# Kernel tuning notes

Measured on AMD Instinct MI355X. Metric: run time of the kernel, lower is better.

The kernel has to match this reference:

```python
import jax, jax.numpy as jnp
import numpy as np

SHIFT_MIN, SHIFT_MAX = -14.0, 0.0  # deepshift range for weight_bits=5: (-(2**4-2), 0)


def shift_quant(w):
    """Quantize weights to signed powers of two (bit-shift weights), STE form."""
    sign = jnp.sign(w)
    shift = jnp.clip(jnp.round(jnp.log2(jnp.abs(w) + 1e-12)), SHIFT_MIN, SHIFT_MAX)
    q = sign * jnp.exp2(shift)
    return w + jax.lax.stop_gradient(q - w)


def moe_fc(t, wg, w0, b0, w1, b1):
    """Top-1 routing over 2 experts: expert0 dense Linear, expert1 shift-quantized Linear.
    t: [T, C]; weights torch-layout [out, in]. With top_k=1 the softmaxed top-k gate is 1.0,
    so combine is a hard select of the chosen expert's output."""
    logits = t @ wg                      # [T, 2]
    pick0 = (jnp.argmax(logits, axis=-1) == 0)[:, None]
    y0 = t @ w0.T + b0                   # dense expert
    y1 = t @ shift_quant(w1).T + b1      # shift expert
    return jnp.where(pick0, y0, y1)


def setup_inputs() -> dict:
    key = jax.random.key(0)
    ks = jax.random.split(key, 10)
    B, N, C, Dh = 16, 1024, 512, 2048
    s = 0.02
    return {
        "x": jax.random.normal(ks[0], (B, N, C), jnp.float32),
        "H": 32,
        "W": 32,
        "wg1": jax.random.normal(ks[1], (C, 2), jnp.float32) * s,
        "fc1_w0": jax.random.normal(ks[2], (Dh, C), jnp.float32) * s,
        "fc1_b0": jnp.zeros((Dh,), jnp.float32),
        "fc1_w1": jax.random.normal(ks[3], (Dh, C), jnp.float32) * s,
        "fc1_b1": jnp.zeros((Dh,), jnp.float32),
        "dw_w": jax.random.normal(ks[4], (Dh, 1, 3, 3), jnp.float32) * np.sqrt(2.0 / 9.0),
        "dw_b": jnp.zeros((Dh,), jnp.float32),
        "wg2": jax.random.normal(ks[5], (Dh, 2), jnp.float32) * s,
        "fc2_w0": jax.random.normal(ks[6], (C, Dh), jnp.float32) * s,
        "fc2_b0": jnp.zeros((C,), jnp.float32),
        "fc2_w1": jax.random.normal(ks[7], (C, Dh), jnp.float32) * s,
        "fc2_b1": jnp.zeros((C,), jnp.float32),
    }


def reference(x, H, W, wg1, fc1_w0, fc1_b0, fc1_w1, fc1_b1, dw_w, dw_b,
              wg2, fc2_w0, fc2_b0, fc2_w1, fc2_b1):
    B, N, C = x.shape
    Dh = fc1_w0.shape[0]
    # fc1 MoE
    h = moe_fc(x.reshape(-1, C), wg1, fc1_w0, fc1_b0, fc1_w1, fc1_b1)  # [B*N, Dh]
    # DWConv 3x3 depthwise, NCHW
    h = h.reshape(B, N, Dh).transpose(0, 2, 1).reshape(B, Dh, H, W)
    h = jax.lax.conv_general_dilated(
        h, dw_w, window_strides=(1, 1), padding="SAME",
        dimension_numbers=("NCHW", "OIHW", "NCHW"), feature_group_count=Dh)
    h = h + dw_b[None, :, None, None]
    h = h.reshape(B, Dh, N).transpose(0, 2, 1)  # [B, N, Dh]
    # GELU (exact, as nn.GELU default); dropout p=0 -> identity
    h = jax.nn.gelu(h, approximate=False)
    # fc2 MoE
    y = moe_fc(h.reshape(-1, Dh), wg2, fc2_w0, fc2_b0, fc2_w1, fc2_b1)
    return y.reshape(B, N, -1)
```

## Files before the change

### kernel.cpp

```cpp
#include <hip/hip_runtime.h>
#include <hip/hip_bf16.h>


#define TOKS  16384
#define CIN   512
#define DHID  2048

typedef __attribute__((ext_vector_type(8))) __bf16 bf16x8;
typedef __attribute__((ext_vector_type(4))) float  f32x4;
typedef __attribute__((ext_vector_type(4))) float  float4v;
typedef __attribute__((ext_vector_type(4))) unsigned short ushort4v;

__device__ __forceinline__ unsigned short f2bf(float f) {
  union { float f; unsigned int u; } a; a.f = f;
  unsigned int u = a.u;
  unsigned int r = u + 0x7FFFu + ((u >> 16) & 1u);
  return (unsigned short)(r >> 16);
}
__device__ __forceinline__ float bf2f(unsigned short h) {
  union { unsigned int u; float f; } a; a.u = ((unsigned int)h) << 16;
  return a.f;
}

__device__ __forceinline__ float squant(float w) {
  if (w == 0.0f) return 0.0f;
  float aw = fabsf(w) + 1e-12f;
  union { float f; unsigned u; } a; a.f = aw;
  int e = (int)((a.u >> 23) & 0xFFu) - 127;
  unsigned frac = a.u & 0x7FFFFFu;
  int shift = e + (frac >= 0x3504F4u ? 1 : 0);
  shift = min(max(shift, -14), 0);
  union { unsigned u; float f; } q; q.u = (unsigned)(shift + 127) << 23;
  return (w > 0.0f) ? q.f : -q.f;
}

#define GLDS16(gp, lp) __builtin_amdgcn_global_load_lds(                      \
    (const __attribute__((address_space(1))) void*)(gp),                      \
    (__attribute__((address_space(3))) void*)(lp), 16, 0, 0)

__global__ void k_prep(const float* __restrict__ w0, const float* __restrict__ w1,
                       const float* __restrict__ w20, const float* __restrict__ w21,
                       unsigned short* __restrict__ w0hi, unsigned short* __restrict__ w0lo,
                       unsigned short* __restrict__ w1q, unsigned short* __restrict__ w20b,
                       unsigned short* __restrict__ w21b) {
  int i = blockIdx.x * 256 + threadIdx.x;
  if (i >= DHID * CIN) return;
  float v = w0[i];
  unsigned short h = f2bf(v);
  w0hi[i] = h;
  w0lo[i] = f2bf(v - bf2f(h));
  w1q[i]  = f2bf(squant(w1[i]));
  w20b[i] = f2bf(w20[i]);
  w21b[i] = f2bf(squant(w21[i]));
}

__global__ void k_prepx(const float* __restrict__ x,
                        unsigned short* __restrict__ xhi, unsigned short* __restrict__ xlo) {
  int i = blockIdx.x * 256 + threadIdx.x;
  float4v v = ((const float4v*)x)[i];
  ushort4v hv, lv;
  #pragma unroll
  for (int q = 0; q < 4; ++q) {
    unsigned short h = f2bf(v[q]);
    hv[q] = h;
    lv[q] = f2bf(v[q] - bf2f(h));
  }
  ((ushort4v*)xhi)[i] = hv;
  ((ushort4v*)xlo)[i] = lv;
}

__global__ void k_gate1(const float* __restrict__ x, const float* __restrict__ wg1,
                        unsigned char* __restrict__ pick1) {
  int tok = blockIdx.x * 4 + (threadIdx.x >> 6);
  int l = threadIdx.x & 63;
  const float* xr = x + (size_t)tok * CIN;
  float s0 = 0.f, s1 = 0.f;
  for (int i = l; i < CIN; i += 64) {
    float v = xr[i];
    s0 += v * wg1[i * 2 + 0];
    s1 += v * wg1[i * 2 + 1];
  }
  for (int m = 32; m; m >>= 1) { s0 += __shfl_xor(s0, m); s1 += __shfl_xor(s1, m); }
  if (l == 0) pick1[tok] = (s0 >= s1) ? 0 : 1;
}

__global__ void k_scan(const unsigned char* __restrict__ pick, int* __restrict__ perm,
                       int* __restrict__ n0buf) {
  __shared__ int cnt[1024];
  const int t = threadIdx.x;
  unsigned char loc[16];
  int c0 = 0;
  #pragma unroll
  for (int i = 0; i < 16; ++i) { loc[i] = pick[t * 16 + i]; c0 += (loc[i] == 0); }
  cnt[t] = c0;
  __syncthreads();
  for (int off = 1; off < 1024; off <<= 1) {
    int v = cnt[t] + ((t >= off) ? cnt[t - off] : 0);
    __syncthreads();
    cnt[t] = v;
    __syncthreads();
  }
  int total0 = cnt[1023];
  int pre0 = cnt[t] - c0;
  int pre1 = t * 16 - pre0;
  if (t == 0) n0buf[0] = total0;
  int p0 = pre0, p1 = total0 + pre1;
  #pragma unroll
  for (int i = 0; i < 16; ++i) {
    int tok = t * 16 + i;
    if (loc[i] == 0) perm[p0++] = tok; else perm[p1++] = tok;
  }
}

__launch_bounds__(256, 2)
__global__ void k_fc1(const unsigned short* __restrict__ xhi,
                      const unsigned short* __restrict__ xlo,
                      const unsigned short* __restrict__ w0hi,
                      const unsigned short* __restrict__ w0lo,
                      const unsigned short* __restrict__ w1q,
                      const float* __restrict__ b0, const float* __restrict__ b1,
                      const int* __restrict__ perm, const int* __restrict__ n0buf,
                      float* __restrict__ h32) {
  __shared__ unsigned short sm[40960];
  const int t = threadIdx.x, wv = t >> 6, ln = t & 63;
  const int lr = ln & 15, lg = ln >> 4;
  const int tok0 = blockIdx.x * 128, nbase = blockIdx.y * 128;
  const int wm = (wv >> 1) * 64, wn = (wv & 1) * 64;
  const int n0 = n0buf[0];
  const bool do0 = (tok0 < n0), do1 = (tok0 + 128 > n0);

  int par[2];
  #pragma unroll
  for (int s = 0; s < 2; ++s)
    par[s] = perm[tok0 + ((s * 4 + wv) << 4) + (ln >> 2)];

  const int swsrc = (((ln & 3) ^ ((ln >> 3) & 3)) << 3);
  const int swrd  = ((lg ^ ((lr >> 1) & 3)) << 3);

  f32x4 acc0[4][4], acc1[4][4];
  #pragma unroll
  for (int i = 0; i < 4; ++i)
    #pragma unroll
    for (int j = 0; j < 4; ++j) {
      acc0[i][j] = f32x4{0.f, 0.f, 0.f, 0.f};
      acc1[i][j] = f32x4{0.f, 0.f, 0.f, 0.f};
    }

  auto STAGE = [&](int kt, int db) {
    const int k0 = kt * 32;
    #pragma unroll
    for (int s = 0; s < 2; ++s) {
      const int rowblk = s * 4 + wv;
      const int aoff = db * 8192 + (rowblk << 9);
      const int boff = 16384 + db * 12288 + (rowblk << 9);
      size_t ga = (size_t)par[s] * CIN + k0 + swsrc;
      size_t gb = (size_t)(nbase + (rowblk << 4) + (ln >> 2)) * CIN + k0 + swsrc;
      GLDS16(xhi + ga, &sm[aoff]);
      GLDS16(xlo + ga, &sm[aoff + 4096]);
      GLDS16(w0hi + gb, &sm[boff]);
      GLDS16(w0lo + gb, &sm[boff + 4096]);
      GLDS16(w1q + gb, &sm[boff + 8192]);
    }
  };

  auto COMPUTE = [&](int db) {
    bf16x8 ah[4], al[4];
    #pragma unroll
    for (int mt = 0; mt < 4; ++mt) {
      int ro = (wm + (mt << 4) + lr) * 32 + swrd;
      ah[mt] = *(const bf16x8*)&sm[db * 8192 + ro];
      al[mt] = *(const bf16x8*)&sm[db * 8192 + 4096 + ro];
    }
    __builtin_amdgcn_s_setprio(1);
    #pragma unroll
    for (int nt = 0; nt < 4; ++nt) {
      int bb = 16384 + db * 12288 + (wn + (nt << 4) + lr) * 32 + swrd;
      if (do0) {
        bf16x8 bh = *(const bf16x8*)&sm[bb];
        bf16x8 bl = *(const bf16x8*)&sm[bb + 4096];
        #pragma unroll
        for (int mt = 0; mt < 4; ++mt) {
          acc0[mt][nt] = __builtin_amdgcn_mfma_f32_16x16x32_bf16(ah[mt], bh, acc0[mt][nt], 0, 0, 0);
          acc0[mt][nt] = __builtin_amdgcn_mfma_f32_16x16x32_bf16(al[mt], bh, acc0[mt][nt], 0, 0, 0);
          acc0[mt][nt] = __builtin_amdgcn_mfma_f32_16x16x32_bf16(ah[mt], bl, acc0[mt][nt], 0, 0, 0);
        }
      }
      if (do1) {
        bf16x8 bq = *(const bf16x8*)&sm[bb + 8192];
        #pragma unroll
        for (int mt = 0; mt < 4; ++mt) {
          acc1[mt][nt] = __builtin_amdgcn_mfma_f32_16x16x32_bf16(ah[mt], bq, acc1[mt][nt], 0, 0, 0);
          acc1[mt][nt] = __builtin_amdgcn_mfma_f32_16x16x32_bf16(al[mt], bq, acc1[mt][nt], 0, 0, 0);
        }
      }
    }
    __builtin_amdgcn_s_setprio(0);
  };

  STAGE(0, 0);
  #pragma unroll 2
  for (int kt = 0; kt < 15; ++kt) {
    __builtin_amdgcn_s_barrier();
    __builtin_amdgcn_sched_barrier(0);
    STAGE(kt + 1, (kt + 1) & 1);
    asm volatile("s_waitcnt vmcnt(10)" ::: "memory");
    __builtin_amdgcn_s_barrier();
    __builtin_amdgcn_sched_barrier(0);
    COMPUTE(kt & 1);
  }
  asm volatile("s_waitcnt vmcnt(0)" ::: "memory");
  __builtin_amdgcn_s_barrier();
  __builtin_amdgcn_sched_barrier(0);
  COMPUTE(1);

  #pragma unroll
  for (int nt = 0; nt < 4; ++nt) {
    int d = nbase + wn + (nt << 4) + lr;
    float bi0 = b0[d], bi1 = b1[d];
    #pragma unroll
    for (int mt = 0; mt < 4; ++mt) {
      f32x4 v0 = acc0[mt][nt], v1 = acc1[mt][nt];
      #pragma unroll
      for (int rr = 0; rr < 4; ++rr) {
        int pos = tok0 + wm + (mt << 4) + (lg << 2) + rr;
        int tok = perm[pos];
        float val = (pos >= n0) ? (v1[rr] + bi1) : (v0[rr] + bi0);
        h32[(size_t)tok * DHID + d] = val;
      }
    }
  }
}

__global__ void k_conv(const float* __restrict__ h32, const float* __restrict__ dww,
                       const float* __restrict__ dwb, const float* __restrict__ wg2,
                       unsigned short* __restrict__ hb, float* __restrict__ part) {
  __shared__ float tile[10][32][32];
  const int dc = blockIdx.x;
  const int ys = blockIdx.y;
  const int b  = blockIdx.z;
  const int t = threadIdx.x;
  const int d0 = dc * 32, y0 = ys * 8;

  for (int p = 0; p < 10240; p += 256) {
    int idx = p + t;
    int dl = idx & 31, xx = (idx >> 5) & 31, ry = idx >> 10;
    int y = y0 - 1 + ry;
    float v = 0.f;
    if (y >= 0 && y < 32)
      v = h32[(size_t)(b * 1024 + y * 32 + xx) * DHID + d0 + dl];
    tile[ry][xx][dl] = v;
  }
  __syncthreads();

  const int dl = t & 31, xg = t >> 5;
  const int d = d0 + dl;
  float kk[9];
  #pragma unroll
  for (int i = 0; i < 9; ++i) kk[i] = dww[d * 9 + i];
  const float bias = dwb[d];
  const float g0 = wg2[d * 2 + 0], g1 = wg2[d * 2 + 1];

  for (int yy = 0; yy < 8; ++yy) {
    int ry = yy + 1;
    #pragma unroll
    for (int xi = 0; xi < 4; ++xi) {
      int xx = xg * 4 + xi;
      float s = bias;
      #pragma unroll
      for (int dy = -1; dy <= 1; ++dy)
        #pragma unroll
        for (int dx = -1; dx <= 1; ++dx) {
          int xs = xx + dx;
          float v = (xs >= 0 && xs < 32) ? tile[ry + dy][xs][dl] : 0.f;
          s += v * kk[(dy + 1) * 3 + (dx + 1)];
        }
      float gg = 0.5f * s * (1.0f + erff(s * 0.70710678118654752f));
      int tok = b * 1024 + (y0 + yy) * 32 + xx;
      hb[(size_t)tok * DHID + d] = f2bf(gg);
      float p0 = gg * g0, p1 = gg * g1;
      for (int m = 16; m; m >>= 1) { p0 += __shfl_xor(p0, m); p1 += __shfl_xor(p1, m); }
      if (dl == 0) {
        part[(size_t)tok * 128 + dc] = p0;
        part[(size_t)tok * 128 + 64 + dc] = p1;
      }
    }
  }
}

__global__ void k_gate2(const float* __restrict__ part, unsigned char* __restrict__ pick2) {
  int tok = blockIdx.x * 4 + (threadIdx.x >> 6);
  int l = threadIdx.x & 63;
  const float* pr = part + (size_t)tok * 128;
  float s0 = pr[l], s1 = pr[64 + l];
  for (int m = 32; m; m >>= 1) { s0 += __shfl_xor(s0, m); s1 += __shfl_xor(s1, m); }
  if (l == 0) pick2[tok] = (s0 >= s1) ? 0 : 1;
}

__launch_bounds__(256, 2)
__global__ void k_fc2(const unsigned short* __restrict__ hb,
                      const unsigned short* __restrict__ w20b,
                      const unsigned short* __restrict__ w21b,
                      const float* __restrict__ b0, const float* __restrict__ b1,
                      const int* __restrict__ perm, const int* __restrict__ n0buf,
                      float* __restrict__ out) {
  __shared__ unsigned short sm[24576];
  const int t = threadIdx.x, wv = t >> 6, ln = t & 63;
  const int lr = ln & 15, lg = ln >> 4;
  const int tok0 = blockIdx.x * 128, nbase = blockIdx.y * 128;
  const int wm = (wv >> 1) * 64, wn = (wv & 1) * 64;
  const int n0 = n0buf[0];
  const bool do0 = (tok0 < n0), do1 = (tok0 + 128 > n0);

  int par[2];
  #pragma unroll
  for (int s = 0; s < 2; ++s)
    par[s] = perm[tok0 + ((s * 4 + wv) << 4) + (ln >> 2)];

  const int swsrc = (((ln & 3) ^ ((ln >> 3) & 3)) << 3);
  const int swrd  = ((lg ^ ((lr >> 1) & 3)) << 3);

  f32x4 acc0[4][4], acc1[4][4];
  #pragma unroll
  for (int i = 0; i < 4; ++i)
    #pragma unroll
    for (int j = 0; j < 4; ++j) {
      acc0[i][j] = f32x4{0.f, 0.f, 0.f, 0.f};
      acc1[i][j] = f32x4{0.f, 0.f, 0.f, 0.f};
    }

  auto STAGE = [&](int kt, int db) {
    const int k0 = kt * 32;
    #pragma unroll
    for (int s = 0; s < 2; ++s) {
      const int rowblk = s * 4 + wv;
      const int aoff = db * 4096 + (rowblk << 9);
      const int boff = 8192 + db * 8192 + (rowblk << 9);
      size_t ga = (size_t)par[s] * DHID + k0 + swsrc;
      size_t gb = (size_t)(nbase + (rowblk << 4) + (ln >> 2)) * DHID + k0 + swsrc;
      GLDS16(hb + ga, &sm[aoff]);
      GLDS16(w20b + gb, &sm[boff]);
      GLDS16(w21b + gb, &sm[boff + 4096]);
    }
  };

  auto COMPUTE = [&](int db) {
    bf16x8 a[4];
    #pragma unroll
    for (int mt = 0; mt < 4; ++mt)
      a[mt] = *(const bf16x8*)&sm[db * 4096 + (wm + (mt << 4) + lr) * 32 + swrd];
    __builtin_amdgcn_s_setprio(1);
    #pragma unroll
    for (int nt = 0; nt < 4; ++nt) {
      int bb = 8192 + db * 8192 + (wn + (nt << 4) + lr) * 32 + swrd;
      if (do0) {
        bf16x8 b0f = *(const bf16x8*)&sm[bb];
        #pragma unroll
        for (int mt = 0; mt < 4; ++mt)
          acc0[mt][nt] = __builtin_amdgcn_mfma_f32_16x16x32_bf16(a[mt], b0f, acc0[mt][nt], 0, 0, 0);
      }
      if (do1) {
        bf16x8 b1f = *(const bf16x8*)&sm[bb + 4096];
        #pragma unroll
        for (int mt = 0; mt < 4; ++mt)
          acc1[mt][nt] = __builtin_amdgcn_mfma_f32_16x16x32_bf16(a[mt], b1f, acc1[mt][nt], 0, 0, 0);
      }
    }
    __builtin_amdgcn_s_setprio(0);
  };

  STAGE(0, 0);
  #pragma unroll 2
  for (int kt = 0; kt < 63; ++kt) {
    __builtin_amdgcn_s_barrier();
    __builtin_amdgcn_sched_barrier(0);
    STAGE(kt + 1, (kt + 1) & 1);
    asm volatile("s_waitcnt vmcnt(6)" ::: "memory");
    __builtin_amdgcn_s_barrier();
    __builtin_amdgcn_sched_barrier(0);
    COMPUTE(kt & 1);
  }
  asm volatile("s_waitcnt vmcnt(0)" ::: "memory");
  __builtin_amdgcn_s_barrier();
  __builtin_amdgcn_sched_barrier(0);
  COMPUTE(1);

  #pragma unroll
  for (int nt = 0; nt < 4; ++nt) {
    int c = nbase + wn + (nt << 4) + lr;
    float bi0 = b0[c], bi1 = b1[c];
    #pragma unroll
    for (int mt = 0; mt < 4; ++mt) {
      f32x4 v0 = acc0[mt][nt], v1 = acc1[mt][nt];
      #pragma unroll
      for (int rr = 0; rr < 4; ++rr) {
        int pos = tok0 + wm + (mt << 4) + (lg << 2) + rr;
        int tok = perm[pos];
        float val = (pos >= n0) ? (v1[rr] + bi1) : (v0[rr] + bi0);
        out[(size_t)tok * CIN + c] = val;
      }
    }
  }
}

extern "C" void kernel_launch(void* const* d_in, const int* in_sizes, int n_in,
                              void* d_out, int out_size, void* d_ws, size_t ws_size,
                              hipStream_t stream) {
  (void)in_sizes; (void)n_in; (void)out_size; (void)ws_size;
  const float* x   = (const float*)d_in[0];
  const float* wg1 = (const float*)d_in[3];
  const float* w0  = (const float*)d_in[4];
  const float* b0  = (const float*)d_in[5];
  const float* w1  = (const float*)d_in[6];
  const float* b1  = (const float*)d_in[7];
  const float* dww = (const float*)d_in[8];
  const float* dwb = (const float*)d_in[9];
  const float* wg2 = (const float*)d_in[10];
  const float* w20 = (const float*)d_in[11];
  const float* b20 = (const float*)d_in[12];
  const float* w21 = (const float*)d_in[13];
  const float* b21 = (const float*)d_in[14];
  float* out = (float*)d_out;

  char* ws = (char*)d_ws;
  const size_t MB2 = 1u << 21;
  unsigned short* w0hi = (unsigned short*)(ws + 0 * MB2);
  unsigned short* w0lo = (unsigned short*)(ws + 1 * MB2);
  unsigned short* w1q  = (unsigned short*)(ws + 2 * MB2);
  unsigned short* w20b = (unsigned short*)(ws + 3 * MB2);
  unsigned short* w21b = (unsigned short*)(ws + 4 * MB2);
  char* p = ws + 5 * MB2;
  unsigned short* xhi = (unsigned short*)p;            p += (size_t)TOKS * CIN * 2;
  unsigned short* xlo = (unsigned short*)p;            p += (size_t)TOKS * CIN * 2;
  unsigned char* pick1 = (unsigned char*)p;            p += 65536;
  unsigned char* pick2 = (unsigned char*)p;            p += 65536;
  int* perm1 = (int*)p;                                p += TOKS * 4;
  int* perm2 = (int*)p;                                p += TOKS * 4;
  int* n0a   = (int*)p;                                p += 256;
  int* n0b   = (int*)p;                                p += 256;
  float* part = (float*)p;                             p += (size_t)TOKS * 128 * 4;
  float* h32  = (float*)p;                             p += (size_t)TOKS * DHID * 4;
  unsigned short* hb = (unsigned short*)p;

  k_prep <<<4096, 256, 0, stream>>>(w0, w1, w20, w21, w0hi, w0lo, w1q, w20b, w21b);
  k_prepx<<<8192, 256, 0, stream>>>(x, xhi, xlo);
  k_gate1<<<4096, 256, 0, stream>>>(x, wg1, pick1);
  k_scan <<<1, 1024, 0, stream>>>(pick1, perm1, n0a);
  k_fc1  <<<dim3(128, 16), 256, 0, stream>>>(xhi, xlo, w0hi, w0lo, w1q, b0, b1, perm1, n0a, h32);
  k_conv <<<dim3(64, 4, 16), 256, 0, stream>>>(h32, dww, dwb, wg2, hb, part);
  k_gate2<<<4096, 256, 0, stream>>>(part, pick2);
  k_scan <<<1, 1024, 0, stream>>>(pick2, perm2, n0b);
  k_fc2  <<<dim3(128, 4), 256, 0, stream>>>(hb, w20b, w21b, b20, b21, perm2, n0b, out);
}
```

Measured before the change: 441.7 us.

## Stage GEMM epilogues through LDS, vectorize conv, and swizzle block order

The fc1 and fc2 epilogues now write the accumulators into shared memory and read them back, so each row of scattered output goes to global memory as 16-byte vector stores instead of 4-byte strided scalar stores. The depthwise conv kernel is rewritten so each thread handles four channels, loading and storing them as float4 and bf16x4 vectors, and the gate partial reduction needs fewer shuffles. The GEMM grids become 1D with a grouped block ordering (8 token tiles per group) to improve L2 reuse of the weight tiles. This adds an extra LDS round trip and a __syncthreads in each epilogue.

```diff
diff --git a/kernel.cpp b/kernel.cpp
--- a/kernel.cpp
+++ b/kernel.cpp
@@ -124,7 +124,9 @@
   __shared__ unsigned short sm[40960];
   const int t = threadIdx.x, wv = t >> 6, ln = t & 63;
   const int lr = ln & 15, lg = ln >> 4;
-  const int tok0 = blockIdx.x * 128, nbase = blockIdx.y * 128;
+  const int g = blockIdx.x, q = g >> 3;
+  const int tok0 = ((g & 7) + ((q >> 4) << 3)) * 128;
+  const int nbase = (q & 15) * 128;
   const int wm = (wv >> 1) * 64, wn = (wv & 1) * 64;
   const int n0 = n0buf[0];
   const bool do0 = (tok0 < n0), do1 = (tok0 + 128 > n0);
@@ -213,76 +215,101 @@
   __builtin_amdgcn_sched_barrier(0);
   COMPUTE(1);
 
+  __syncthreads();
+  float* smf = (float*)sm;
+  float bi0[4], bi1[4];
   #pragma unroll
   for (int nt = 0; nt < 4; ++nt) {
     int d = nbase + wn + (nt << 4) + lr;
-    float bi0 = b0[d], bi1 = b1[d];
-    #pragma unroll
-    for (int mt = 0; mt < 4; ++mt) {
+    bi0[nt] = b0[d]; bi1[nt] = b1[d];
+  }
+  #pragma unroll
+  for (int mt = 0; mt < 4; ++mt) {
+    #pragma unroll
+    for (int nt = 0; nt < 4; ++nt) {
       f32x4 v0 = acc0[mt][nt], v1 = acc1[mt][nt];
       #pragma unroll
       for (int rr = 0; rr < 4; ++rr) {
         int pos = tok0 + wm + (mt << 4) + (lg << 2) + rr;
-        int tok = perm[pos];
-        float val = (pos >= n0) ? (v1[rr] + bi1) : (v0[rr] + bi0);
-        h32[(size_t)tok * DHID + d] = val;
-      }
-    }
-  }
-}
-
+        float val = (pos >= n0) ? (v1[rr] + bi1[nt]) : (v0[rr] + bi0[nt]);
+        smf[wv * 1088 + ((lg << 2) + rr) * 68 + (nt << 4) + lr] = val;
+      }
+    }
+    #pragma unroll
+    for (int p = 0; p < 4; ++p) {
+      int row = (p << 2) + (ln >> 4);
+      f32x4 vv = *(const f32x4*)&smf[wv * 1088 + row * 68 + ((ln & 15) << 2)];
+      int tok = perm[tok0 + wm + (mt << 4) + row];
+      *(f32x4*)&h32[(size_t)tok * DHID + nbase + wn + ((ln & 15) << 2)] = vv;
+    }
+  }
+}
+
+__launch_bounds__(256)
 __global__ void k_conv(const float* __restrict__ h32, const float* __restrict__ dww,
                        const float* __restrict__ dwb, const float* __restrict__ wg2,
                        unsigned short* __restrict__ hb, float* __restrict__ part) {
-  __shared__ float tile[10][32][32];
+  __shared__ float4v tile[10][32][8];
   const int dc = blockIdx.x;
   const int ys = blockIdx.y;
   const int b  = blockIdx.z;
   const int t = threadIdx.x;
   const int d0 = dc * 32, y0 = ys * 8;
-
-  for (int p = 0; p < 10240; p += 256) {
-    int idx = p + t;
-    int dl = idx & 31, xx = (idx >> 5) & 31, ry = idx >> 10;
+  const int dl4 = t & 7, xq = t >> 3;
+
+  #pragma unroll
+  for (int ry = 0; ry < 10; ++ry) {
     int y = y0 - 1 + ry;
-    float v = 0.f;
+    float4v v = {0.f, 0.f, 0.f, 0.f};
     if (y >= 0 && y < 32)
-      v = h32[(size_t)(b * 1024 + y * 32 + xx) * DHID + d0 + dl];
-    tile[ry][xx][dl] = v;
+      v = *(const float4v*)&h32[(size_t)(b * 1024 + y * 32 + xq) * DHID + d0 + dl4 * 4];
+    tile[ry][xq][dl4] = v;
   }
   __syncthreads();
 
-  const int dl = t & 31, xg = t >> 5;
-  const int d = d0 + dl;
-  float kk[9];
-  #pragma unroll
-  for (int i = 0; i < 9; ++i) kk[i] = dww[d * 9 + i];
-  const float bias = dwb[d];
-  const float g0 = wg2[d * 2 + 0], g1 = wg2[d * 2 + 1];
-
+  const int d = d0 + dl4 * 4;
+  float4v kk[9];
+  #pragma unroll
+  for (int i = 0; i < 9; ++i) {
+    kk[i][0] = dww[(d + 0) * 9 + i]; kk[i][1] = dww[(d + 1) * 9 + i];
+    kk[i][2] = dww[(d + 2) * 9 + i]; kk[i][3] = dww[(d + 3) * 9 + i];
+  }
+  const float4v bias = *(const float4v*)&dwb[d];
+  float4v g0v, g1v;
+  #pragma unroll
+  for (int j = 0; j < 4; ++j) { g0v[j] = wg2[(d + j) * 2]; g1v[j] = wg2[(d + j) * 2 + 1]; }
+
+  #pragma unroll
   for (int yy = 0; yy < 8; ++yy) {
-    int ry = yy + 1;
-    #pragma unroll
-    for (int xi = 0; xi < 4; ++xi) {
-      int xx = xg * 4 + xi;
-      float s = bias;
+    float4v s = bias;
+    #pragma unroll
+    for (int dy = 0; dy < 3; ++dy)
       #pragma unroll
-      for (int dy = -1; dy <= 1; ++dy)
-        #pragma unroll
-        for (int dx = -1; dx <= 1; ++dx) {
-          int xs = xx + dx;
-          float v = (xs >= 0 && xs < 32) ? tile[ry + dy][xs][dl] : 0.f;
-          s += v * kk[(dy + 1) * 3 + (dx + 1)];
+      for (int dx = 0; dx < 3; ++dx) {
+        int xs = xq + dx - 1;
+        if (xs >= 0 && xs < 32) {
+          float4v v = tile[yy + dy][xs][dl4];
+          float4v k = kk[dy * 3 + dx];
+          s[0] += v[0] * k[0]; s[1] += v[1] * k[1];
+          s[2] += v[2] * k[2]; s[3] += v[3] * k[3];
         }
-      float gg = 0.5f * s * (1.0f + erff(s * 0.70710678118654752f));
-      int tok = b * 1024 + (y0 + yy) * 32 + xx;
-      hb[(size_t)tok * DHID + d] = f2bf(gg);
-      float p0 = gg * g0, p1 = gg * g1;
-      for (int m = 16; m; m >>= 1) { p0 += __shfl_xor(p0, m); p1 += __shfl_xor(p1, m); }
-      if (dl == 0) {
-        part[(size_t)tok * 128 + dc] = p0;
-        part[(size_t)tok * 128 + 64 + dc] = p1;
-      }
+      }
+    float4v gg;
+    #pragma unroll
+    for (int j = 0; j < 4; ++j)
+      gg[j] = 0.5f * s[j] * (1.0f + erff(s[j] * 0.70710678118654752f));
+    int tok = b * 1024 + (y0 + yy) * 32 + xq;
+    ushort4v hv;
+    #pragma unroll
+    for (int j = 0; j < 4; ++j) hv[j] = f2bf(gg[j]);
+    *(ushort4v*)&hb[(size_t)tok * DHID + d] = hv;
+    float p0 = gg[0] * g0v[0] + gg[1] * g0v[1] + gg[2] * g0v[2] + gg[3] * g0v[3];
+    float p1 = gg[0] * g1v[0] + gg[1] * g1v[1] + gg[2] * g1v[2] + gg[3] * g1v[3];
+    p0 += __shfl_xor(p0, 1); p0 += __shfl_xor(p0, 2); p0 += __shfl_xor(p0, 4);
+    p1 += __shfl_xor(p1, 1); p1 += __shfl_xor(p1, 2); p1 += __shfl_xor(p1, 4);
+    if (dl4 == 0) {
+      part[(size_t)tok * 128 + dc] = p0;
+      part[(size_t)tok * 128 + 64 + dc] = p1;
     }
   }
 }
@@ -306,7 +333,9 @@
   __shared__ unsigned short sm[24576];
   const int t = threadIdx.x, wv = t >> 6, ln = t & 63;
   const int lr = ln & 15, lg = ln >> 4;
-  const int tok0 = blockIdx.x * 128, nbase = blockIdx.y * 128;
+  const int g = blockIdx.x, q = g >> 3;
+  const int tok0 = ((g & 7) + ((q >> 2) << 3)) * 128;
+  const int nbase = (q & 3) * 128;
   const int wm = (wv >> 1) * 64, wn = (wv & 1) * 64;
   const int n0 = n0buf[0];
   const bool do0 = (tok0 < n0), do1 = (tok0 + 128 > n0);
@@ -384,20 +413,32 @@
   __builtin_amdgcn_sched_barrier(0);
   COMPUTE(1);
 
+  __syncthreads();
+  float* smf = (float*)sm;
+  float bi0[4], bi1[4];
   #pragma unroll
   for (int nt = 0; nt < 4; ++nt) {
     int c = nbase + wn + (nt << 4) + lr;
-    float bi0 = b0[c], bi1 = b1[c];
-    #pragma unroll
-    for (int mt = 0; mt < 4; ++mt) {
+    bi0[nt] = b0[c]; bi1[nt] = b1[c];
+  }
+  #pragma unroll
+  for (int mt = 0; mt < 4; ++mt) {
+    #pragma unroll
+    for (int nt = 0; nt < 4; ++nt) {
       f32x4 v0 = acc0[mt][nt], v1 = acc1[mt][nt];
       #pragma unroll
       for (int rr = 0; rr < 4; ++rr) {
         int pos = tok0 + wm + (mt << 4) + (lg << 2) + rr;
-        int tok = perm[pos];
-        float val = (pos >= n0) ? (v1[rr] + bi1) : (v0[rr] + bi0);
-        out[(size_t)tok * CIN + c] = val;
-      }
+        float val = (pos >= n0) ? (v1[rr] + bi1[nt]) : (v0[rr] + bi0[nt]);
+        smf[wv * 1088 + ((lg << 2) + rr) * 68 + (nt << 4) + lr] = val;
+      }
+    }
+    #pragma unroll
+    for (int p = 0; p < 4; ++p) {
+      int row = (p << 2) + (ln >> 4);
+      f32x4 vv = *(const f32x4*)&smf[wv * 1088 + row * 68 + ((ln & 15) << 2)];
+      int tok = perm[tok0 + wm + (mt << 4) + row];
+      *(f32x4*)&out[(size_t)tok * CIN + nbase + wn + ((ln & 15) << 2)] = vv;
     }
   }
 }
@@ -445,9 +486,9 @@
   k_prepx<<<8192, 256, 0, stream>>>(x, xhi, xlo);
   k_gate1<<<4096, 256, 0, stream>>>(x, wg1, pick1);
   k_scan <<<1, 1024, 0, stream>>>(pick1, perm1, n0a);
-  k_fc1  <<<dim3(128, 16), 256, 0, stream>>>(xhi, xlo, w0hi, w0lo, w1q, b0, b1, perm1, n0a, h32);
+  k_fc1  <<<2048, 256, 0, stream>>>(xhi, xlo, w0hi, w0lo, w1q, b0, b1, perm1, n0a, h32);
   k_conv <<<dim3(64, 4, 16), 256, 0, stream>>>(h32, dww, dwb, wg2, hb, part);
   k_gate2<<<4096, 256, 0, stream>>>(part, pick2);
   k_scan <<<1, 1024, 0, stream>>>(pick2, perm2, n0b);
-  k_fc2  <<<dim3(128, 4), 256, 0, stream>>>(hb, w20b, w21b, b20, b21, perm2, n0b, out);
-}
+  k_fc2  <<<512, 256, 0, stream>>>(hb, w20b, w21b, b20, b21, perm2, n0b, out);
+}
```

Result: faster. 424.6 us (-3.9%).
